# Kernel tuning notes

Measured on AMD Instinct MI355X. Metric: run time of the kernel, lower is better.

Reference implementation:

```python
import jax, jax.numpy as jnp
import numpy as np

LN_EPS = 1e-5

def _layer_norm(x):
    m = jnp.mean(x, axis=-1, keepdims=True)
    v = jnp.mean(jnp.square(x - m), axis=-1, keepdims=True)
    return (x - m) / jnp.sqrt(v + LN_EPS)

def setup_inputs() -> dict:
    key = jax.random.key(0)
    ks = jax.random.split(key, 6)
    B, S, d_in, d_out = 8, 2048, 1024, 4096
    x = jax.random.normal(ks[0], (B, S, d_in), dtype=jnp.float32)
    # torch.randn % 1 -> values in [0, 1)
    weight_in = jax.random.uniform(ks[1], (d_out, d_in), dtype=jnp.float32)
    bias_in = jax.random.uniform(ks[2], (d_out,), dtype=jnp.float32)
    weight_out = jax.random.uniform(ks[3], (d_in, d_out), dtype=jnp.float32)
    bias_out = jax.random.uniform(ks[4], (d_in,), dtype=jnp.float32)
    lengths = jax.random.randint(ks[5], (B,), 1, S + 1, dtype=jnp.int64 if jax.config.read('jax_enable_x64') else jnp.int32)
    return {"x": x, "weight_in": weight_in, "bias_in": bias_in,
            "weight_out": weight_out, "bias_out": bias_out, "lengths": lengths}

def reference(x, weight_in, bias_in, weight_out, bias_out, lengths):
    # lengths is unused mathematically in the dense baseline (ragged kernels
    # only skip padded rows; valid-region math identical).
    for _ in range(10):
        x = jnp.einsum('bsd,od->bso', x, weight_in) + bias_in  # [B,S,d_out]
        x = _layer_norm(x)
        x = jnp.einsum('bso,do->bsd', x, weight_out) + bias_out  # [B,S,d_in]
        x = _layer_norm(x)
    return x
```

## Files before the change

### kernel.cpp

```cpp
#include <hip/hip_runtime.h>


typedef __attribute__((ext_vector_type(4))) float f32x4;
typedef __attribute__((ext_vector_type(8))) __bf16 bf16x8;

#define LN_EPS 1e-5f

__device__ __forceinline__ ushort f2bf(float f) {
    union { float f; uint u; } c; c.f = f;
    uint u = c.u;
    uint r = (u + 0x7fffu + ((u >> 16) & 1u)) >> 16;
    return (ushort)r;
}

typedef const __attribute__((address_space(1))) void* gas_ptr;
typedef __attribute__((address_space(3))) void* las_ptr;

__device__ __forceinline__ void gload_lds16(const void* g, void* l) {
    __builtin_amdgcn_global_load_lds((gas_ptr)g, (las_ptr)l, 16, 0, 0);
}

__device__ __forceinline__ bf16x8 ldf(const ushort* base, int byteoff) {
    return *reinterpret_cast<const bf16x8*>(
        reinterpret_cast<const char*>(base) + byteoff);
}

__global__ __launch_bounds__(256) void conv_f32_bf16(
        const float* __restrict__ in, ushort* __restrict__ outp, int n4) {
    int i = blockIdx.x * 256 + threadIdx.x;
    if (i >= n4) return;
    float4 f = reinterpret_cast<const float4*>(in)[i];
    ushort4 r;
    r.x = f2bf(f.x); r.y = f2bf(f.y); r.z = f2bf(f.z); r.w = f2bf(f.w);
    reinterpret_cast<ushort4*>(outp)[i] = r;
}

template<int M, int N, int K>
__global__ __launch_bounds__(512)
void gemm256_8ph(const ushort* __restrict__ A, const ushort* __restrict__ B,
                 const float* __restrict__ bias, ushort* __restrict__ C) {
    constexpr int NT  = K / 64;
    constexpr int NIT = NT / 2;
    constexpr int NBX = N / 256;
    constexpr int NWG = (M / 256) * NBX;

    __shared__ __attribute__((aligned(16))) ushort lds[2][2][2][8192];

    const int tid  = threadIdx.x;
    const int wid  = tid >> 6;
    const int lane = tid & 63;
    const int wr   = wid >> 2;
    const int wc   = wid & 3;

    int bn0, bm0;
    if constexpr (NBX == 16) {
        const int x = blockIdx.x & 7, j = blockIdx.x >> 3;
        bn0 = (x * 2 + (j & 1)) * 256;
        bm0 = (j >> 1) * 256;
    } else {
        int bid = (blockIdx.x & 7) * (NWG >> 3) + (blockIdx.x >> 3);
        bn0 = (bid % NBX) * 256;
        bm0 = (bid / NBX) * 256;
    }

    const int trow = tid >> 3;
    const int cg   = (tid & 7) ^ (trow & 7);
    const ushort* Asrc = A + (size_t)(bm0 + trow) * K + cg * 8;
    const ushort* Bsrc = B + (size_t)(bn0 + trow) * K + cg * 8;

    const int fr  = lane & 15;
    const int fq  = lane >> 4;
    const int s8  = lane & 7;
    const int cb0 = ((fq       ^ s8) << 4);
    const int cb1 = (((4 + fq) ^ s8) << 4);
    const int brb = (wc & 1) * 64;

    const ushort* Ah[2] = { &lds[0][0][wr][0],      &lds[1][0][wr][0] };
    const ushort* Bh[2] = { &lds[0][1][wc >> 1][0], &lds[1][1][wc >> 1][0] };

    f32x4 acc[8][4] = {};
    bf16x8 aLo[4][2], aHi[4][2], bLo[2][2], bHi[2][2];

#define STAGE_A(buf, h, kts) do { \
    gload_lds16(Asrc + (size_t)((h)*128     ) * K + (kts), (void*)&lds[buf][0][h][       wid*512]); \
    gload_lds16(Asrc + (size_t)((h)*128 + 64) * K + (kts), (void*)&lds[buf][0][h][4096 + wid*512]); } while(0)
#define STAGE_B(buf, h, kts) do { \
    gload_lds16(Bsrc + (size_t)((h)*128     ) * K + (kts), (void*)&lds[buf][1][h][       wid*512]); \
    gload_lds16(Bsrc + (size_t)((h)*128 + 64) * K + (kts), (void*)&lds[buf][1][h][4096 + wid*512]); } while(0)

#define READ_ALO(b) do { _Pragma("unroll") for (int i = 0; i < 4; ++i) { \
    aLo[i][0] = ldf(Ah[b], (i*16+fr)*128 + cb0); \
    aLo[i][1] = ldf(Ah[b], (i*16+fr)*128 + cb1); } } while(0)
#define READ_AHI(b) do { _Pragma("unroll") for (int i = 0; i < 4; ++i) { \
    aHi[i][0] = ldf(Ah[b], ((i+4)*16+fr)*128 + cb0); \
    aHi[i][1] = ldf(Ah[b], ((i+4)*16+fr)*128 + cb1); } } while(0)
#define READ_BLO(b) do { _Pragma("unroll") for (int j = 0; j < 2; ++j) { \
    bLo[j][0] = ldf(Bh[b], (brb + j*16 + fr)*128 + cb0); \
    bLo[j][1] = ldf(Bh[b], (brb + j*16 + fr)*128 + cb1); } } while(0)
#define READ_BHI(b) do { _Pragma("unroll") for (int j = 0; j < 2; ++j) { \
    bHi[j][0] = ldf(Bh[b], (brb + (j+2)*16 + fr)*128 + cb0); \
    bHi[j][1] = ldf(Bh[b], (brb + (j+2)*16 + fr)*128 + cb1); } } while(0)

#define MFMA_BLK(AF, ioff, BF, joff) do { \
    _Pragma("unroll") for (int i = 0; i < 4; ++i) \
    _Pragma("unroll") for (int j = 0; j < 2; ++j) { \
        acc[i+ioff][j+joff] = __builtin_amdgcn_mfma_f32_16x16x32_bf16(AF[i][0], BF[j][0], acc[i+ioff][j+joff], 0, 0, 0); \
        acc[i+ioff][j+joff] = __builtin_amdgcn_mfma_f32_16x16x32_bf16(AF[i][1], BF[j][1], acc[i+ioff][j+joff], 0, 0, 0); } } while(0)

#define BARRIER() __builtin_amdgcn_s_barrier()
#define VMCNT4()  asm volatile("s_waitcnt vmcnt(4)" ::: "memory")

    STAGE_B(0, 0, 0);  STAGE_B(0, 1, 0);
    STAGE_A(0, 0, 0);  STAGE_A(0, 1, 0);
    STAGE_B(1, 0, 64); STAGE_B(1, 1, 64);
    VMCNT4();
    BARRIER();

    for (int it = 0; it < NIT; ++it) {
        const int k1 = it * 128 + 64;
        const int k2 = (it * 128 + 128) & (K - 1);
        const int k3 = (it * 128 + 192) & (K - 1);

        READ_ALO(0); READ_BLO(0);
        STAGE_A(1, 0, k1);
        BARRIER();
        __builtin_amdgcn_s_setprio(1); MFMA_BLK(aLo, 0, bLo, 0); __builtin_amdgcn_s_setprio(0);
        BARRIER();
        READ_BHI(0);
        STAGE_A(1, 1, k1);
        BARRIER();
        __builtin_amdgcn_s_setprio(1); MFMA_BLK(aLo, 0, bHi, 2); __builtin_amdgcn_s_setprio(0);
        BARRIER();
        READ_AHI(0);
        STAGE_B(0, 0, k2);
        BARRIER();
        __builtin_amdgcn_s_setprio(1); MFMA_BLK(aHi, 4, bLo, 0); __builtin_amdgcn_s_setprio(0);
        BARRIER();
        STAGE_B(0, 1, k2);
        BARRIER();
        __builtin_amdgcn_s_setprio(1); MFMA_BLK(aHi, 4, bHi, 2); __builtin_amdgcn_s_setprio(0);
        VMCNT4();
        BARRIER();
        READ_ALO(1); READ_BLO(1);
        STAGE_A(0, 0, k2);
        BARRIER();
        __builtin_amdgcn_s_setprio(1); MFMA_BLK(aLo, 0, bLo, 0); __builtin_amdgcn_s_setprio(0);
        BARRIER();
        READ_BHI(1);
        STAGE_A(0, 1, k2);
        BARRIER();
        __builtin_amdgcn_s_setprio(1); MFMA_BLK(aLo, 0, bHi, 2); __builtin_amdgcn_s_setprio(0);
        BARRIER();
        READ_AHI(1);
        STAGE_B(1, 0, k3);
        BARRIER();
        __builtin_amdgcn_s_setprio(1); MFMA_BLK(aHi, 4, bLo, 0); __builtin_amdgcn_s_setprio(0);
        BARRIER();
        STAGE_B(1, 1, k3);
        BARRIER();
        __builtin_amdgcn_s_setprio(1); MFMA_BLK(aHi, 4, bHi, 2); __builtin_amdgcn_s_setprio(0);
        VMCNT4();
        BARRIER();
    }

    asm volatile("s_waitcnt vmcnt(0)" ::: "memory");
    __syncthreads();

    ushort* eps = (ushort*)&lds[0][0][0][0];
    #pragma unroll
    for (int j = 0; j < 4; ++j) {
        const int c  = wc * 64 + j * 16 + fr;
        const float bv = bias[bn0 + c];
        #pragma unroll
        for (int i = 0; i < 8; ++i) {
            const int rbase = wr * 128 + i * 16;
            #pragma unroll
            for (int q = 0; q < 4; ++q) {
                const int rloc = rbase + fq * 4 + q;
                const int csw  = c ^ (((rloc >> 2) & 3) << 4);
                eps[rloc * 256 + csw] = f2bf(acc[i][j][q] + bv);
            }
        }
    }
    __syncthreads();

    {
        const int g  = tid >> 4;
        const int q4 = (tid >> 2) & 3;
        const int a  = tid & 3;
        const int rb = (g >> 2) * 16 + q4 * 4 + (g & 3);
        const int keyx = q4 << 4;
        #pragma unroll
        for (int h = 0; h < 2; ++h) {
            const int r = rb + h * 128;
            const ushort* rp = eps + r * 256;
            ushort* cp = C + (size_t)(bm0 + r) * N + bn0;
            #pragma unroll
            for (int k = 0; k < 8; ++k) {
                const int col = (4 * k + a) * 8;
                *reinterpret_cast<uint4*>(cp + col) =
                    *reinterpret_cast<const uint4*>(rp + (col ^ keyx));
            }
        }
    }
#undef STAGE_A
#undef STAGE_B
#undef READ_ALO
#undef READ_AHI
#undef READ_BLO
#undef READ_BHI
#undef MFMA_BLK
#undef BARRIER
#undef VMCNT4
}

template<int W, bool F32OUT>
__global__ __launch_bounds__(256)
void ln_rows(ushort* __restrict__ y, float* __restrict__ outp) {
    constexpr int NIT = W / 512;
    const int wid  = threadIdx.x >> 6;
    const int lane = threadIdx.x & 63;
    const size_t row = (size_t)blockIdx.x * 4 + wid;
    ushort* p = y + row * W;

    bf16x8 v[NIT];
    float sum = 0.f, sumsq = 0.f;
    #pragma unroll
    for (int i = 0; i < NIT; ++i) {
        v[i] = *reinterpret_cast<const bf16x8*>(p + i * 512 + lane * 8);
        #pragma unroll
        for (int j = 0; j < 8; ++j) {
            const float f = (float)v[i][j];
            sum += f; sumsq += f * f;
        }
    }
    #pragma unroll
    for (int off = 32; off > 0; off >>= 1) {
        sum   += __shfl_xor(sum, off);
        sumsq += __shfl_xor(sumsq, off);
    }
    const float mean = sum * (1.0f / W);
    const float var  = fmaxf(sumsq * (1.0f / W) - mean * mean, 0.f);
    const float rstd = rsqrtf(var + LN_EPS);

    #pragma unroll
    for (int i = 0; i < NIT; ++i) {
        if constexpr (F32OUT) {
            float* op = outp + row * W + i * 512 + lane * 8;
            float4 o0, o1;
            o0.x = ((float)v[i][0] - mean) * rstd;
            o0.y = ((float)v[i][1] - mean) * rstd;
            o0.z = ((float)v[i][2] - mean) * rstd;
            o0.w = ((float)v[i][3] - mean) * rstd;
            o1.x = ((float)v[i][4] - mean) * rstd;
            o1.y = ((float)v[i][5] - mean) * rstd;
            o1.z = ((float)v[i][6] - mean) * rstd;
            o1.w = ((float)v[i][7] - mean) * rstd;
            reinterpret_cast<float4*>(op)[0] = o0;
            reinterpret_cast<float4*>(op)[1] = o1;
        } else {
            ushort4 r0, r1;
            r0.x = f2bf(((float)v[i][0] - mean) * rstd);
            r0.y = f2bf(((float)v[i][1] - mean) * rstd);
            r0.z = f2bf(((float)v[i][2] - mean) * rstd);
            r0.w = f2bf(((float)v[i][3] - mean) * rstd);
            r1.x = f2bf(((float)v[i][4] - mean) * rstd);
            r1.y = f2bf(((float)v[i][5] - mean) * rstd);
            r1.z = f2bf(((float)v[i][6] - mean) * rstd);
            r1.w = f2bf(((float)v[i][7] - mean) * rstd);
            ushort* op = p + i * 512 + lane * 8;
            reinterpret_cast<ushort4*>(op)[0] = r0;
            reinterpret_cast<ushort4*>(op)[1] = r1;
        }
    }
}

extern "C" void kernel_launch(void* const* d_in, const int* in_sizes, int n_in,
                              void* d_out, int out_size, void* d_ws, size_t ws_size,
                              hipStream_t stream) {
    const float* x     = (const float*)d_in[0];
    const float* w_in  = (const float*)d_in[1];
    const float* b_in  = (const float*)d_in[2];
    const float* w_out = (const float*)d_in[3];
    const float* b_out = (const float*)d_in[4];

    constexpr int Mrows = 16384;
    constexpr int Din   = 1024;
    constexpr int Dout  = 4096;

    char* ws = (char*)d_ws;
    ushort* wib = (ushort*)ws;  ws += (size_t)Dout * Din * 2;
    ushort* wob = (ushort*)ws;  ws += (size_t)Din * Dout * 2;
    ushort* xb  = (ushort*)ws;  ws += (size_t)Mrows * Din * 2;
    ushort* yb  = (ushort*)ws;

    const dim3 blk(256);

    conv_f32_bf16<<<(Dout * Din / 4) / 256, blk, 0, stream>>>(w_in,  wib, Dout * Din / 4);
    conv_f32_bf16<<<(Din * Dout / 4) / 256, blk, 0, stream>>>(w_out, wob, Din * Dout / 4);
    conv_f32_bf16<<<(Mrows * Din / 4) / 256, blk, 0, stream>>>(x, xb, Mrows * Din / 4);

    for (int it = 0; it < 10; ++it) {
        gemm256_8ph<Mrows, Dout, Din>
            <<<(Mrows / 256) * (Dout / 256), dim3(512), 0, stream>>>(xb, wib, b_in, yb);
        ln_rows<Dout, false><<<Mrows / 4, blk, 0, stream>>>(yb, nullptr);
        gemm256_8ph<Mrows, Din, Dout>
            <<<(Mrows / 256) * (Din / 256), dim3(512), 0, stream>>>(yb, wob, b_out, xb);
        if (it < 9) {
            ln_rows<Din, false><<<Mrows / 4, blk, 0, stream>>>(xb, nullptr);
        } else {
            ln_rows<Din, true><<<Mrows / 4, blk, 0, stream>>>(xb, (float*)d_out);
        }
    }
}
```

Measured before the change: 2.952 ms.

## Fold LayerNorm into GEMM epilogue via weight row sums and partial stats

Replaces the separate normalize-in-place LayerNorm passes with algebra: the next GEMM consumes un-normalized activations and applies rstd*acc - rstd*mean*rowsum(W) + bias in its epilogue, using precomputed weight row sums. The epilogue also emits per-tile partial sum and sum-of-squares, which a small reduce kernel turns into per-row mean and rstd. This removes the read-modify-write of the large intermediates. It also switches from bf16 to fp16 storage and MFMA, which changes the numerical range and precision, and the one-pass variance formula on un-normalized values risks cancellation.

```diff
diff --git a/kernel.cpp b/kernel.cpp
--- a/kernel.cpp
+++ b/kernel.cpp
@@ -1,16 +1,14 @@
 #include <hip/hip_runtime.h>
 
 
-typedef __attribute__((ext_vector_type(4))) float f32x4;
-typedef __attribute__((ext_vector_type(8))) __bf16 bf16x8;
+typedef __attribute__((ext_vector_type(4))) float    f32x4;
+typedef __attribute__((ext_vector_type(8))) _Float16 f16x8;
+typedef __attribute__((ext_vector_type(4))) _Float16 f16x4;
 
 #define LN_EPS 1e-5f
 
-__device__ __forceinline__ ushort f2bf(float f) {
-    union { float f; uint u; } c; c.f = f;
-    uint u = c.u;
-    uint r = (u + 0x7fffu + ((u >> 16) & 1u)) >> 16;
-    return (ushort)r;
+__device__ __forceinline__ ushort f2h_bits(float f) {
+    union { _Float16 h; ushort u; } c; c.h = (_Float16)f; return c.u;
 }
 
 typedef const __attribute__((address_space(1))) void* gas_ptr;
@@ -20,31 +18,82 @@
     __builtin_amdgcn_global_load_lds((gas_ptr)g, (las_ptr)l, 16, 0, 0);
 }
 
-__device__ __forceinline__ bf16x8 ldf(const ushort* base, int byteoff) {
-    return *reinterpret_cast<const bf16x8*>(
+__device__ __forceinline__ f16x8 ldf(const _Float16* base, int byteoff) {
+    return *reinterpret_cast<const f16x8*>(
         reinterpret_cast<const char*>(base) + byteoff);
 }
 
-__global__ __launch_bounds__(256) void conv_f32_bf16(
-        const float* __restrict__ in, ushort* __restrict__ outp, int n4) {
+__global__ __launch_bounds__(256) void conv_f32_f16(
+        const float* __restrict__ in, _Float16* __restrict__ outp, int n4) {
     int i = blockIdx.x * 256 + threadIdx.x;
     if (i >= n4) return;
     float4 f = reinterpret_cast<const float4*>(in)[i];
-    ushort4 r;
-    r.x = f2bf(f.x); r.y = f2bf(f.y); r.z = f2bf(f.z); r.w = f2bf(f.w);
-    reinterpret_cast<ushort4*>(outp)[i] = r;
+    f16x4 r;
+    r[0] = (_Float16)f.x; r[1] = (_Float16)f.y;
+    r[2] = (_Float16)f.z; r[3] = (_Float16)f.w;
+    *reinterpret_cast<f16x4*>(&outp[(size_t)i * 4]) = r;
+}
+
+template<int W>
+__global__ __launch_bounds__(256)
+void rowsum_rows(const _Float16* __restrict__ w, float* __restrict__ outp) {
+    const int wid  = threadIdx.x >> 6;
+    const int lane = threadIdx.x & 63;
+    const size_t row = (size_t)blockIdx.x * 4 + wid;
+    const _Float16* p = w + row * W;
+    float s = 0.f;
+    #pragma unroll
+    for (int i = 0; i < W / 512; ++i) {
+        f16x8 v = *reinterpret_cast<const f16x8*>(p + i * 512 + lane * 8);
+        #pragma unroll
+        for (int j = 0; j < 8; ++j) s += (float)v[j];
+    }
+    #pragma unroll
+    for (int off = 32; off > 0; off >>= 1) s += __shfl_xor(s, off);
+    if (lane == 0) outp[row] = s;
+}
+
+__global__ __launch_bounds__(256) void init_ident_stats(float2* __restrict__ st) {
+    int i = blockIdx.x * 256 + threadIdx.x;
+    st[i] = make_float2(0.f, 1.f);
+}
+
+template<int NP, int W>
+__global__ __launch_bounds__(256)
+void reduce_stats(const float2* __restrict__ part, float2* __restrict__ st) {
+    const int wid  = threadIdx.x >> 6;
+    const int lane = threadIdx.x & 63;
+    const size_t row = (size_t)blockIdx.x * 4 + wid;
+    float s = 0.f, q = 0.f;
+    if (lane < NP) {
+        float2 p = part[row * NP + lane];
+        s = p.x; q = p.y;
+    }
+    #pragma unroll
+    for (int off = 32; off > 0; off >>= 1) {
+        s += __shfl_xor(s, off);
+        q += __shfl_xor(q, off);
+    }
+    if (lane == 0) {
+        const float mean = s * (1.0f / W);
+        const float var  = fmaxf(q * (1.0f / W) - mean * mean, 0.f);
+        st[row] = make_float2(mean, rsqrtf(var + LN_EPS));
+    }
 }
 
 template<int M, int N, int K>
 __global__ __launch_bounds__(512)
-void gemm256_8ph(const ushort* __restrict__ A, const ushort* __restrict__ B,
-                 const float* __restrict__ bias, ushort* __restrict__ C) {
+void gemm256_ln(const _Float16* __restrict__ A, const _Float16* __restrict__ B,
+                const float* __restrict__ bias, const float* __restrict__ wsum,
+                const float2* __restrict__ stats, _Float16* __restrict__ C,
+                float2* __restrict__ partials) {
     constexpr int NT  = K / 64;
     constexpr int NIT = NT / 2;
     constexpr int NBX = N / 256;
     constexpr int NWG = (M / 256) * NBX;
-
-    __shared__ __attribute__((aligned(16))) ushort lds[2][2][2][8192];
+    constexpr int NPART = NBX * 4;
+
+    __shared__ __attribute__((aligned(16))) _Float16 lds[2][2][2][8192];
 
     const int tid  = threadIdx.x;
     const int wid  = tid >> 6;
@@ -65,8 +114,8 @@
 
     const int trow = tid >> 3;
     const int cg   = (tid & 7) ^ (trow & 7);
-    const ushort* Asrc = A + (size_t)(bm0 + trow) * K + cg * 8;
-    const ushort* Bsrc = B + (size_t)(bn0 + trow) * K + cg * 8;
+    const _Float16* Asrc = A + (size_t)(bm0 + trow) * K + cg * 8;
+    const _Float16* Bsrc = B + (size_t)(bn0 + trow) * K + cg * 8;
 
     const int fr  = lane & 15;
     const int fq  = lane >> 4;
@@ -75,11 +124,11 @@
     const int cb1 = (((4 + fq) ^ s8) << 4);
     const int brb = (wc & 1) * 64;
 
-    const ushort* Ah[2] = { &lds[0][0][wr][0],      &lds[1][0][wr][0] };
-    const ushort* Bh[2] = { &lds[0][1][wc >> 1][0], &lds[1][1][wc >> 1][0] };
+    const _Float16* Ah[2] = { &lds[0][0][wr][0],      &lds[1][0][wr][0] };
+    const _Float16* Bh[2] = { &lds[0][1][wc >> 1][0], &lds[1][1][wc >> 1][0] };
 
     f32x4 acc[8][4] = {};
-    bf16x8 aLo[4][2], aHi[4][2], bLo[2][2], bHi[2][2];
+    f16x8 aLo[4][2], aHi[4][2], bLo[2][2], bHi[2][2];
 
 #define STAGE_A(buf, h, kts) do { \
     gload_lds16(Asrc + (size_t)((h)*128     ) * K + (kts), (void*)&lds[buf][0][h][       wid*512]); \
@@ -104,8 +153,8 @@
 #define MFMA_BLK(AF, ioff, BF, joff) do { \
     _Pragma("unroll") for (int i = 0; i < 4; ++i) \
     _Pragma("unroll") for (int j = 0; j < 2; ++j) { \
-        acc[i+ioff][j+joff] = __builtin_amdgcn_mfma_f32_16x16x32_bf16(AF[i][0], BF[j][0], acc[i+ioff][j+joff], 0, 0, 0); \
-        acc[i+ioff][j+joff] = __builtin_amdgcn_mfma_f32_16x16x32_bf16(AF[i][1], BF[j][1], acc[i+ioff][j+joff], 0, 0, 0); } } while(0)
+        acc[i+ioff][j+joff] = __builtin_amdgcn_mfma_f32_16x16x32_f16(AF[i][0], BF[j][0], acc[i+ioff][j+joff], 0, 0, 0); \
+        acc[i+ioff][j+joff] = __builtin_amdgcn_mfma_f32_16x16x32_f16(AF[i][1], BF[j][1], acc[i+ioff][j+joff], 0, 0, 0); } } while(0)
 
 #define BARRIER() __builtin_amdgcn_s_barrier()
 #define VMCNT4()  asm volatile("s_waitcnt vmcnt(4)" ::: "memory")
@@ -166,20 +215,39 @@
     asm volatile("s_waitcnt vmcnt(0)" ::: "memory");
     __syncthreads();
 
+    float bcol[4], wcol[4];
+    #pragma unroll
+    for (int j = 0; j < 4; ++j) {
+        const int c = bn0 + wc * 64 + j * 16 + fr;
+        bcol[j] = bias[c];
+        wcol[j] = wsum[c];
+    }
+
     ushort* eps = (ushort*)&lds[0][0][0][0];
     #pragma unroll
-    for (int j = 0; j < 4; ++j) {
-        const int c  = wc * 64 + j * 16 + fr;
-        const float bv = bias[bn0 + c];
+    for (int i = 0; i < 8; ++i) {
         #pragma unroll
-        for (int i = 0; i < 8; ++i) {
-            const int rbase = wr * 128 + i * 16;
+        for (int q = 0; q < 4; ++q) {
+            const int rloc = wr * 128 + i * 16 + fq * 4 + q;
+            const float2 st = stats[bm0 + rloc];
+            const float rs = st.y, coef = st.y * st.x;
+            const int key = (((rloc >> 2) & 3) << 4);
+            float s = 0.f, sq = 0.f;
             #pragma unroll
-            for (int q = 0; q < 4; ++q) {
-                const int rloc = rbase + fq * 4 + q;
-                const int csw  = c ^ (((rloc >> 2) & 3) << 4);
-                eps[rloc * 256 + csw] = f2bf(acc[i][j][q] + bv);
+            for (int j = 0; j < 4; ++j) {
+                const float v = rs * acc[i][j][q] - coef * wcol[j] + bcol[j];
+                s += v; sq += v * v;
+                const int c = wc * 64 + j * 16 + fr;
+                eps[rloc * 256 + (c ^ key)] = f2h_bits(v);
             }
+            #pragma unroll
+            for (int off = 1; off < 16; off <<= 1) {
+                s  += __shfl_xor(s,  off);
+                sq += __shfl_xor(sq, off);
+            }
+            if (fr == 0)
+                partials[(size_t)(bm0 + rloc) * NPART + (bn0 >> 8) * 4 + wc] =
+                    make_float2(s, sq);
         }
     }
     __syncthreads();
@@ -194,11 +262,11 @@
         for (int h = 0; h < 2; ++h) {
             const int r = rb + h * 128;
             const ushort* rp = eps + r * 256;
-            ushort* cp = C + (size_t)(bm0 + r) * N + bn0;
+            _Float16* cp = C + (size_t)(bm0 + r) * N + bn0;
             #pragma unroll
             for (int k = 0; k < 8; ++k) {
                 const int col = (4 * k + a) * 8;
-                *reinterpret_cast<uint4*>(cp + col) =
+                *reinterpret_cast<uint4*>((ushort*)cp + col) =
                     *reinterpret_cast<const uint4*>(rp + (col ^ keyx));
             }
         }
@@ -214,64 +282,30 @@
 #undef VMCNT4
 }
 
-template<int W, bool F32OUT>
 __global__ __launch_bounds__(256)
-void ln_rows(ushort* __restrict__ y, float* __restrict__ outp) {
-    constexpr int NIT = W / 512;
+void ln_final(const _Float16* __restrict__ a, const float2* __restrict__ st,
+              float* __restrict__ outp) {
     const int wid  = threadIdx.x >> 6;
     const int lane = threadIdx.x & 63;
     const size_t row = (size_t)blockIdx.x * 4 + wid;
-    ushort* p = y + row * W;
-
-    bf16x8 v[NIT];
-    float sum = 0.f, sumsq = 0.f;
-    #pragma unroll
-    for (int i = 0; i < NIT; ++i) {
-        v[i] = *reinterpret_cast<const bf16x8*>(p + i * 512 + lane * 8);
-        #pragma unroll
-        for (int j = 0; j < 8; ++j) {
-            const float f = (float)v[i][j];
-            sum += f; sumsq += f * f;
-        }
-    }
-    #pragma unroll
-    for (int off = 32; off > 0; off >>= 1) {
-        sum   += __shfl_xor(sum, off);
-        sumsq += __shfl_xor(sumsq, off);
-    }
-    const float mean = sum * (1.0f / W);
-    const float var  = fmaxf(sumsq * (1.0f / W) - mean * mean, 0.f);
-    const float rstd = rsqrtf(var + LN_EPS);
-
-    #pragma unroll
-    for (int i = 0; i < NIT; ++i) {
-        if constexpr (F32OUT) {
-            float* op = outp + row * W + i * 512 + lane * 8;
-            float4 o0, o1;
-            o0.x = ((float)v[i][0] - mean) * rstd;
-            o0.y = ((float)v[i][1] - mean) * rstd;
-            o0.z = ((float)v[i][2] - mean) * rstd;
-            o0.w = ((float)v[i][3] - mean) * rstd;
-            o1.x = ((float)v[i][4] - mean) * rstd;
-            o1.y = ((float)v[i][5] - mean) * rstd;
-            o1.z = ((float)v[i][6] - mean) * rstd;
-            o1.w = ((float)v[i][7] - mean) * rstd;
-            reinterpret_cast<float4*>(op)[0] = o0;
-            reinterpret_cast<float4*>(op)[1] = o1;
-        } else {
-            ushort4 r0, r1;
-            r0.x = f2bf(((float)v[i][0] - mean) * rstd);
-            r0.y = f2bf(((float)v[i][1] - mean) * rstd);
-            r0.z = f2bf(((float)v[i][2] - mean) * rstd);
-            r0.w = f2bf(((float)v[i][3] - mean) * rstd);
-            r1.x = f2bf(((float)v[i][4] - mean) * rstd);
-            r1.y = f2bf(((float)v[i][5] - mean) * rstd);
-            r1.z = f2bf(((float)v[i][6] - mean) * rstd);
-            r1.w = f2bf(((float)v[i][7] - mean) * rstd);
-            ushort* op = p + i * 512 + lane * 8;
-            reinterpret_cast<ushort4*>(op)[0] = r0;
-            reinterpret_cast<ushort4*>(op)[1] = r1;
-        }
+    const float2 s = st[row];
+    const float mean = s.x, rstd = s.y;
+    const _Float16* p = a + row * 1024;
+    #pragma unroll
+    for (int i = 0; i < 2; ++i) {
+        f16x8 v = *reinterpret_cast<const f16x8*>(p + i * 512 + lane * 8);
+        float* op = outp + row * 1024 + i * 512 + lane * 8;
+        float4 o0, o1;
+        o0.x = ((float)v[0] - mean) * rstd;
+        o0.y = ((float)v[1] - mean) * rstd;
+        o0.z = ((float)v[2] - mean) * rstd;
+        o0.w = ((float)v[3] - mean) * rstd;
+        o1.x = ((float)v[4] - mean) * rstd;
+        o1.y = ((float)v[5] - mean) * rstd;
+        o1.z = ((float)v[6] - mean) * rstd;
+        o1.w = ((float)v[7] - mean) * rstd;
+        reinterpret_cast<float4*>(op)[0] = o0;
+        reinterpret_cast<float4*>(op)[1] = o1;
     }
 }
 
@@ -289,27 +323,35 @@
     constexpr int Dout  = 4096;
 
     char* ws = (char*)d_ws;
-    ushort* wib = (ushort*)ws;  ws += (size_t)Dout * Din * 2;
-    ushort* wob = (ushort*)ws;  ws += (size_t)Din * Dout * 2;
-    ushort* xb  = (ushort*)ws;  ws += (size_t)Mrows * Din * 2;
-    ushort* yb  = (ushort*)ws;
+    _Float16* wib = (_Float16*)ws; ws += (size_t)Dout * Din * 2;
+    _Float16* wob = (_Float16*)ws; ws += (size_t)Din * Dout * 2;
+    _Float16* a2b = (_Float16*)ws; ws += (size_t)Mrows * Din * 2;
+    _Float16* a1b = (_Float16*)ws; ws += (size_t)Mrows * Dout * 2;
+    float* winsum  = (float*)ws;   ws += Dout * 4;
+    float* woutsum = (float*)ws;   ws += Din * 4;
+    float2* st1 = (float2*)ws;     ws += (size_t)Mrows * 8;
+    float2* st2 = (float2*)ws;     ws += (size_t)Mrows * 8;
+    float2* p1  = (float2*)ws;     ws += (size_t)Mrows * 64 * 8;
+    float2* p2  = (float2*)ws;
 
     const dim3 blk(256);
 
-    conv_f32_bf16<<<(Dout * Din / 4) / 256, blk, 0, stream>>>(w_in,  wib, Dout * Din / 4);
-    conv_f32_bf16<<<(Din * Dout / 4) / 256, blk, 0, stream>>>(w_out, wob, Din * Dout / 4);
-    conv_f32_bf16<<<(Mrows * Din / 4) / 256, blk, 0, stream>>>(x, xb, Mrows * Din / 4);
+    conv_f32_f16<<<(Dout * Din / 4) / 256, blk, 0, stream>>>(w_in,  wib, Dout * Din / 4);
+    conv_f32_f16<<<(Din * Dout / 4) / 256, blk, 0, stream>>>(w_out, wob, Din * Dout / 4);
+    conv_f32_f16<<<(Mrows * Din / 4) / 256, blk, 0, stream>>>(x, a2b, Mrows * Din / 4);
+    rowsum_rows<Din> <<<Dout / 4, blk, 0, stream>>>(wib, winsum);
+    rowsum_rows<Dout><<<Din / 4,  blk, 0, stream>>>(wob, woutsum);
+    init_ident_stats<<<Mrows / 128, blk, 0, stream>>>(st2);
 
     for (int it = 0; it < 10; ++it) {
-        gemm256_8ph<Mrows, Dout, Din>
-            <<<(Mrows / 256) * (Dout / 256), dim3(512), 0, stream>>>(xb, wib, b_in, yb);
-        ln_rows<Dout, false><<<Mrows / 4, blk, 0, stream>>>(yb, nullptr);
-        gemm256_8ph<Mrows, Din, Dout>
-            <<<(Mrows / 256) * (Din / 256), dim3(512), 0, stream>>>(yb, wob, b_out, xb);
-        if (it < 9) {
-            ln_rows<Din, false><<<Mrows / 4, blk, 0, stream>>>(xb, nullptr);
-        } else {
-            ln_rows<Din, true><<<Mrows / 4, blk, 0, stream>>>(xb, (float*)d_out);
-        }
-    }
-}
+        gemm256_ln<Mrows, Dout, Din>
+            <<<(Mrows / 256) * (Dout / 256), dim3(512), 0, stream>>>(
+                a2b, wib, b_in, winsum, st2, a1b, p1);
+        reduce_stats<64, Dout><<<Mrows / 4, blk, 0, stream>>>(p1, st1);
+        gemm256_ln<Mrows, Din, Dout>
+            <<<(Mrows / 256) * (Din / 256), dim3(512), 0, stream>>>(
+                a1b, wob, b_out, woutsum, st1, a2b, p2);
+        reduce_stats<16, Din><<<Mrows / 4, blk, 0, stream>>>(p2, st2);
+    }
+    ln_final<<<Mrows / 4, blk, 0, stream>>>(a2b, st2, (float*)d_out);
+}
```

Measured after the change: 3.058 ms. +3.6%, slower.
